# Performance work log

Hardware: AMD Instinct MI355X
Metric: run time of the kernel (lower is better)

The kernel has to match this reference:

```python
import jax, jax.numpy as jnp
import numpy as np

EPS = 1e-5
NEG_SLOPE = 0.01  # torch F.leaky_relu default


def _batchnorm(h, gamma, beta):
    # BatchNorm1d in training mode: batch stats over node dim, biased variance
    mu = jnp.mean(h, axis=0)
    var = jnp.mean((h - mu) ** 2, axis=0)
    return gamma * (h - mu) * jax.lax.rsqrt(var + EPS) + beta


def setup_inputs() -> dict:
    N, E, H, ED = 16384, 524288, 128, 16
    key = jax.random.key(0)
    ks = jax.random.split(key, 12)
    s = 1.0 / np.sqrt(H)
    return {
        "x": jax.random.normal(ks[0], (N, H), jnp.float32),
        "edge_index": jax.random.randint(ks[1], (2, E), 0, N, jnp.int64),
        "edge_attr": jax.random.normal(ks[2], (E, ED), jnp.float32),
        "Wq": jax.random.normal(ks[3], (H, H), jnp.float32) * s,
        "bq": jnp.zeros((H,), jnp.float32),
        "Wk": jax.random.normal(ks[4], (H, H), jnp.float32) * s,
        "bk": jnp.zeros((H,), jnp.float32),
        "Wv": jax.random.normal(ks[5], (H, H), jnp.float32) * s,
        "bv": jnp.zeros((H,), jnp.float32),
        "We": jax.random.normal(ks[6], (ED, 1), jnp.float32) * (1.0 / np.sqrt(ED)),
        "be": jnp.zeros((1,), jnp.float32),
        "bn1_g": jnp.ones((H,), jnp.float32),
        "bn1_b": jnp.zeros((H,), jnp.float32),
        "W1": jax.random.normal(ks[7], (H, 2 * H), jnp.float32) * s,
        "b1": jnp.zeros((2 * H,), jnp.float32),
        "W2": jax.random.normal(ks[8], (2 * H, H), jnp.float32) * (1.0 / np.sqrt(2 * H)),
        "b2": jnp.zeros((H,), jnp.float32),
        "bn2_g": jnp.ones((H,), jnp.float32),
        "bn2_b": jnp.zeros((H,), jnp.float32),
    }


def reference(x, edge_index, edge_attr, Wq, bq, Wk, bk, Wv, bv, We, be,
              bn1_g, bn1_b, W1, b1, W2, b2, bn2_g, bn2_b):
    N = x.shape[0]
    Q = x @ Wq + bq  # [N, H]
    K = x @ Wk + bk
    V = x @ Wv + bv
    Ebias = (edge_attr @ We + be)[:, 0]  # [E], num_heads == 1
    src, dst = edge_index[0], edge_index[1]
    # per-edge dot product over the FULL hidden dim (as in the source)
    scores = jnp.sum(Q[src] * K[dst], axis=1) + Ebias  # [E]
    scores = jnp.where(scores >= 0, scores, NEG_SLOPE * scores)
    # to_dense_adj scatter-adds edge_attr into a dense [N, N] adjacency
    adj = jnp.zeros((N, N), x.dtype).at[src, dst].add(scores)
    attn = jax.nn.softmax(adj, axis=1)  # dense softmax incl. zero non-edges
    x_new = attn @ V  # [N, H]
    h = _batchnorm(x + x_new, bn1_g, bn1_b)
    ffn = jax.nn.relu(h @ W1 + b1) @ W2 + b2
    return _batchnorm(h + ffn, bn2_g, bn2_b)
```

## Files before the change

kernel.cpp:

```cpp
#include <hip/hip_runtime.h>
#include <hip/hip_bf16.h>
#include <math.h>

#define H 128
#define H2 256
#define SLAB 96
#define LDA 136
#define LDA2 264
#define EPS 1e-5f

typedef __attribute__((ext_vector_type(8))) short s16x8;
typedef __attribute__((ext_vector_type(4))) float f32x4;

__device__ __forceinline__ unsigned short f2bf(float f) {
  unsigned u = __float_as_uint(f);
  unsigned r = (u + 0x7FFFu + ((u >> 16) & 1u)) >> 16;
  return (unsigned short)r;
}
__device__ __forceinline__ float bf2f(unsigned short s) {
  return __uint_as_float(((unsigned)s) << 16);
}
__device__ __forceinline__ unsigned short f2h(float f) {
  union { unsigned short s; _Float16 h; } c; c.h = (_Float16)f; return c.s;
}
__device__ __forceinline__ float h2f(unsigned short u) {
  union { unsigned short s; _Float16 h; } c; c.s = u; return (float)c.h;
}

__global__ void wprep(const float* __restrict__ Wq, const float* __restrict__ Wk,
                      const float* __restrict__ Wv, const float* __restrict__ W1,
                      const float* __restrict__ W2,
                      short* qh, short* ql, short* kh, short* kl,
                      short* vh, short* w1h, short* w2h,
                      int* __restrict__ cnt, float* __restrict__ stats, int N)
{
  int job = blockIdx.z;
  if (job == 5) {
    int t = blockIdx.x * 256 + threadIdx.x;
    if (t < N) cnt[t] = 0;
    if (t < 72 * H) stats[t] = 0.f;
    return;
  }
  const float* src; short* dh; short* dl = nullptr; int Kd, Nn;
  if (job == 0)      { src = Wq; dh = qh;  dl = ql; Kd = 128; Nn = 128; }
  else if (job == 1) { src = Wk; dh = kh;  dl = kl; Kd = 128; Nn = 128; }
  else if (job == 2) { src = Wv; dh = vh;           Kd = 128; Nn = 128; }
  else if (job == 3) { src = W1; dh = w1h;          Kd = 128; Nn = 256; }
  else               { src = W2; dh = w2h;          Kd = 256; Nn = 128; }
  int t = blockIdx.x * 256 + threadIdx.x;
  if (t >= Kd * Nn) return;
  int n = t / Kd, k = t - n * Kd;
  float v = src[(size_t)k * Nn + n];
  unsigned short h = f2bf(v);
  dh[t] = (short)h;
  if (dl) dl[t] = (short)f2bf(v - bf2f(h));
}

__global__ __launch_bounds__(256) void ebias(
    const float* __restrict__ ea, const float* __restrict__ We,
    const float* __restrict__ be, float* __restrict__ Eb, int E)
{
  int e = blockIdx.x * 256 + threadIdx.x;
  if (e >= E) return;
  float4 w0 = *(const float4*)&We[0], w1 = *(const float4*)&We[4];
  float4 w2 = *(const float4*)&We[8], w3 = *(const float4*)&We[12];
  const float4* p = (const float4*)&ea[(size_t)e * 16];
  float4 a0 = p[0], a1 = p[1], a2 = p[2], a3 = p[3];
  float s = a0.x * w0.x + a0.y * w0.y + a0.z * w0.z + a0.w * w0.w
          + a1.x * w1.x + a1.y * w1.y + a1.z * w1.z + a1.w * w1.w
          + a2.x * w2.x + a2.y * w2.y + a2.z * w2.z + a2.w * w2.w
          + a3.x * w3.x + a3.y * w3.y + a3.z * w3.z + a3.w * w3.w;
  Eb[e] = s + be[0];
}

__global__ __launch_bounds__(256) void qkv_mfma(
    const float* __restrict__ x,
    const short* __restrict__ Wqh, const short* __restrict__ Wql,
    const short* __restrict__ Wkh, const short* __restrict__ Wkl,
    const short* __restrict__ Wvh,
    const float* __restrict__ bq, const float* __restrict__ bk,
    const float* __restrict__ bv,
    unsigned short* __restrict__ Qh, unsigned short* __restrict__ Kh,
    unsigned short* __restrict__ Vh, float* __restrict__ SVp)
{
  __shared__ __align__(16) short Ahi[64 * LDA];
  __shared__ __align__(16) short Alo[64 * LDA];
  int tid = threadIdx.x;
  int bm = blockIdx.x * 64;
  int wave = tid >> 6, lane = tid & 63;
  int quad = lane >> 4, l16 = lane & 15;
  int wn = wave * 32;

#pragma unroll
  for (int i = 0; i < 4; ++i) {
    int g = i * 256 + tid;
    int row = g >> 4, f = g & 15;
    const float4* xp = (const float4*)&x[(size_t)(bm + row) * H + f * 8];
    float4 v0 = xp[0], v1 = xp[1];
    float vv[8] = {v0.x, v0.y, v0.z, v0.w, v1.x, v1.y, v1.z, v1.w};
    s16x8 hv, lv;
#pragma unroll
    for (int j = 0; j < 8; ++j) {
      unsigned short hh = f2bf(vv[j]);
      hv[j] = (short)hh;
      lv[j] = (short)f2bf(vv[j] - bf2f(hh));
    }
    *(s16x8*)&Ahi[row * LDA + f * 8] = hv;
    *(s16x8*)&Alo[row * LDA + f * 8] = lv;
  }
  __syncthreads();

  for (int ph = 0; ph < 3; ++ph) {
    const short* Bh = (ph == 0) ? Wqh : (ph == 1) ? Wkh : Wvh;
    const short* Bl = (ph == 0) ? Wql : (ph == 1) ? Wkl : nullptr;

    s16x8 bh[2][4], bl2[2][4];
#pragma unroll
    for (int nt = 0; nt < 2; ++nt)
#pragma unroll
      for (int ks = 0; ks < 4; ++ks)
        bh[nt][ks] = *(const s16x8*)&Bh[(size_t)(wn + nt * 16 + l16) * H + ks * 32 + quad * 8];
    if (Bl) {
#pragma unroll
      for (int nt = 0; nt < 2; ++nt)
#pragma unroll
        for (int ks = 0; ks < 4; ++ks)
          bl2[nt][ks] = *(const s16x8*)&Bl[(size_t)(wn + nt * 16 + l16) * H + ks * 32 + quad * 8];
    }

    f32x4 acc[4][2];
#pragma unroll
    for (int mt = 0; mt < 4; ++mt)
#pragma unroll
      for (int nt = 0; nt < 2; ++nt) acc[mt][nt] = (f32x4){0.f, 0.f, 0.f, 0.f};

#pragma unroll
    for (int ks = 0; ks < 4; ++ks) {
      int kof = ks * 32 + quad * 8;
      s16x8 ah[4], al[4];
#pragma unroll
      for (int mt = 0; mt < 4; ++mt) {
        ah[mt] = *(s16x8*)&Ahi[(mt * 16 + l16) * LDA + kof];
        al[mt] = *(s16x8*)&Alo[(mt * 16 + l16) * LDA + kof];
      }
#pragma unroll
      for (int mt = 0; mt < 4; ++mt)
#pragma unroll
        for (int nt = 0; nt < 2; ++nt) {
          acc[mt][nt] = __builtin_amdgcn_mfma_f32_16x16x32_bf16(ah[mt], bh[nt][ks], acc[mt][nt], 0, 0, 0);
          if (ph < 2) {
            acc[mt][nt] = __builtin_amdgcn_mfma_f32_16x16x32_bf16(ah[mt], bl2[nt][ks], acc[mt][nt], 0, 0, 0);
            acc[mt][nt] = __builtin_amdgcn_mfma_f32_16x16x32_bf16(al[mt], bh[nt][ks], acc[mt][nt], 0, 0, 0);
          }
        }
    }

    if (ph == 0) {
#pragma unroll
      for (int nt = 0; nt < 2; ++nt) {
        int col = wn + nt * 16 + l16;
        float bb = bq[col];
#pragma unroll
        for (int mt = 0; mt < 4; ++mt)
#pragma unroll
          for (int r = 0; r < 4; ++r) {
            int row = bm + mt * 16 + quad * 4 + r;
            Qh[(size_t)row * H + col] = f2h(acc[mt][nt][r] + bb);
          }
      }
    } else if (ph == 1) {
#pragma unroll
      for (int nt = 0; nt < 2; ++nt) {
        int col = wn + nt * 16 + l16;
        float bb = bk[col];
#pragma unroll
        for (int mt = 0; mt < 4; ++mt)
#pragma unroll
          for (int r = 0; r < 4; ++r) {
            int row = bm + mt * 16 + quad * 4 + r;
            Kh[(size_t)row * H + col] = f2h(acc[mt][nt][r] + bb);
          }
      }
    } else {
      int bank = blockIdx.x & 7;
#pragma unroll
      for (int nt = 0; nt < 2; ++nt) {
        int col = wn + nt * 16 + l16;
        float bb = bv[col];
        float ps = 0.f;
#pragma unroll
        for (int mt = 0; mt < 4; ++mt)
#pragma unroll
          for (int r = 0; r < 4; ++r) {
            int row = bm + mt * 16 + quad * 4 + r;
            float v = acc[mt][nt][r] + bb;
            Vh[(size_t)row * H + col] = f2h(v);
            ps += v;
          }
        ps += __shfl_xor(ps, 16);
        ps += __shfl_xor(ps, 32);
        if (quad == 0) atomicAdd(&SVp[bank * H + col], ps);
      }
    }
  }
}

__global__ __launch_bounds__(256) void ebfill(
    const int* __restrict__ ei,
    const float* __restrict__ Eb,
    const unsigned short* __restrict__ Qh,
    const unsigned short* __restrict__ Kh,
    int* __restrict__ cnt,
    int2* __restrict__ slabDE, int E, int N)
{
  __shared__ int qeP[2048];
  __shared__ float qeB[2048];
  __shared__ int qn;
  int tid = threadIdx.x;
  int grp = blockIdx.x & 7;
  int blk = blockIdx.x >> 3;
  int lo = grp * (N >> 3), hi = lo + (N >> 3);
  int per = E >> 8;
  int base = blk * per;
  const int* eiD = ei + E;

  if (tid == 0) qn = 0;
  __syncthreads();

  for (int i = 0; i < per; i += 256) {
    int e = base + i + tid;
    if (e >= E) continue;
    int src = ei[e];
    int dst = eiD[e];
    float b = Eb[e];
    if (src >= lo && src < hi) {
      int p = atomicAdd(&qn, 1);
      qeP[p] = (dst << 11) | (src - lo);
      qeB[p] = b;
    }
  }
  __syncthreads();

  int m = qn;
  int sub = tid & 7, st = tid >> 3;
  int j = st;
  for (; j + 32 < m; j += 64) {
    int pA = qeP[j], pB = qeP[j + 32];
    float bA = qeB[j], bB = qeB[j + 32];
    int sA = lo + (pA & 2047), dA = pA >> 11;
    int sB = lo + (pB & 2047), dB = pB >> 11;
    const s16x8* qpA = (const s16x8*)(Qh + (size_t)sA * H);
    const s16x8* kpA = (const s16x8*)(Kh + (size_t)dA * H);
    const s16x8* qpB = (const s16x8*)(Qh + (size_t)sB * H);
    const s16x8* kpB = (const s16x8*)(Kh + (size_t)dB * H);
    s16x8 qa0 = qpA[sub], qb0 = qpA[8 + sub];
    s16x8 ka0 = kpA[sub], kb0 = kpA[8 + sub];
    s16x8 qa1 = qpB[sub], qb1 = qpB[8 + sub];
    s16x8 ka1 = kpB[sub], kb1 = kpB[8 + sub];
    float s0 = 0.f, s1 = 0.f;
#pragma unroll
    for (int u = 0; u < 8; ++u) {
      s0 += h2f((unsigned short)qa0[u]) * h2f((unsigned short)ka0[u]);
      s0 += h2f((unsigned short)qb0[u]) * h2f((unsigned short)kb0[u]);
      s1 += h2f((unsigned short)qa1[u]) * h2f((unsigned short)ka1[u]);
      s1 += h2f((unsigned short)qb1[u]) * h2f((unsigned short)kb1[u]);
    }
    s0 += __shfl_xor(s0, 1); s1 += __shfl_xor(s1, 1);
    s0 += __shfl_xor(s0, 2); s1 += __shfl_xor(s1, 2);
    s0 += __shfl_xor(s0, 4); s1 += __shfl_xor(s1, 4);
    if (sub == 0) {
      s0 += bA; s1 += bB;
      s0 = (s0 >= 0.f) ? s0 : 0.01f * s0;
      s1 = (s1 >= 0.f) ? s1 : 0.01f * s1;
      int posA = atomicAdd(&cnt[sA], 1);
      if (posA < SLAB) {
        int2 rec; rec.x = dA; rec.y = __float_as_int(s0);
        slabDE[sA * SLAB + posA] = rec;
      }
      int posB = atomicAdd(&cnt[sB], 1);
      if (posB < SLAB) {
        int2 rec; rec.x = dB; rec.y = __float_as_int(s1);
        slabDE[sB * SLAB + posB] = rec;
      }
    }
  }
  for (; j < m; j += 32) {
    int p = qeP[j];
    float b = qeB[j];
    int src = lo + (p & 2047), dst = p >> 11;
    const s16x8* qp = (const s16x8*)(Qh + (size_t)src * H);
    const s16x8* kp = (const s16x8*)(Kh + (size_t)dst * H);
    s16x8 qa = qp[sub], qb = qp[8 + sub];
    s16x8 ka = kp[sub], kb = kp[8 + sub];
    float s = 0.f;
#pragma unroll
    for (int u = 0; u < 8; ++u) {
      s += h2f((unsigned short)qa[u]) * h2f((unsigned short)ka[u]);
      s += h2f((unsigned short)qb[u]) * h2f((unsigned short)kb[u]);
    }
    s += __shfl_xor(s, 1);
    s += __shfl_xor(s, 2);
    s += __shfl_xor(s, 4);
    if (sub == 0) {
      s += b;
      s = (s >= 0.f) ? s : 0.01f * s;
      int pos = atomicAdd(&cnt[src], 1);
      if (pos < SLAB) {
        int2 rec; rec.x = dst; rec.y = __float_as_int(s);
        slabDE[src * SLAB + pos] = rec;
      }
    }
  }
}

__global__ __launch_bounds__(256) void attn_fused(
    const float* __restrict__ x,
    const unsigned short* __restrict__ Vh,
    const float* __restrict__ SVp, const int* __restrict__ cnt,
    const int2* __restrict__ slabDE,
    float* __restrict__ h1, float* __restrict__ sum1p, float* __restrict__ sq1p,
    int N)
{
  __shared__ float sv[4][SLAB];
  __shared__ int sd[4][SLAB];
  __shared__ short sown[4][SLAB];
  __shared__ float csum[H], csq[H];
  int tid = threadIdx.x;
  int team = tid >> 6, lane = tid & 63;
  int i = blockIdx.x * 4 + team;
  int k = cnt[i]; if (k > SLAB) k = SLAB;
  int base = i * SLAB;

  if (tid < H) { csum[tid] = 0.f; csq[tid] = 0.f; }
  __syncthreads();

  for (int p = lane; p < k; p += 64) {
    int2 de = slabDE[base + p];
    sd[team][p] = de.x;
    sv[team][p] = __int_as_float(de.y);
  }

  for (int p = lane; p < k; p += 64) {
    int d = sd[team][p];
    int o = p;
    for (int q = p - 1; q >= 0; --q)
      o = (sd[team][q] == d) ? q : o;
    sown[team][p] = (short)o;
  }
  for (int p = lane; p < k; p += 64) {
    int o = sown[team][p];
    if (o != p) atomicAdd(&sv[team][o], sv[team][p]);
  }

  float mx = 0.f;
  for (int p = lane; p < k; p += 64)
    if (sown[team][p] == (short)p) mx = fmaxf(mx, sv[team][p]);
#pragma unroll
  for (int msk = 32; msk; msk >>= 1) mx = fmaxf(mx, __shfl_xor(mx, msk));
  float em = __expf(-mx);

  float zl = 0.f;
  for (int p = lane; p < k; p += 64) {
    float cf = 0.f;
    if (sown[team][p] == (short)p) cf = __expf(sv[team][p] - mx) - em;
    sv[team][p] = cf;
    zl += cf;
  }
#pragma unroll
  for (int msk = 32; msk; msk >>= 1) zl += __shfl_xor(zl, msk);
  float Zi = 1.f / ((float)N * em + zl);

  float sx = 0.f, sy = 0.f;
#pragma unroll
  for (int b = 0; b < 8; ++b) {
    float2 t = *(const float2*)&SVp[b * H + lane * 2];
    sx += t.x; sy += t.y;
  }

  const ushort2* V2 = (const ushort2*)Vh;
  float ax = em * sx, ay = em * sy;
  int c = 0;
  for (; c + 8 <= k; c += 8) {
    float cf[8]; int dd[8]; ushort2 vv[8];
#pragma unroll
    for (int u = 0; u < 8; ++u) { cf[u] = sv[team][c + u]; dd[u] = sd[team][c + u]; }
#pragma unroll
    for (int u = 0; u < 8; ++u) vv[u] = V2[(size_t)dd[u] * 64 + lane];
#pragma unroll
    for (int u = 0; u < 8; ++u) {
      ax += cf[u] * h2f(vv[u].x);
      ay += cf[u] * h2f(vv[u].y);
    }
  }
  for (; c < k; ++c) {
    float cf = sv[team][c];
    ushort2 v0 = V2[(size_t)sd[team][c] * 64 + lane];
    ax += cf * h2f(v0.x); ay += cf * h2f(v0.y);
  }
  float2 xx = *(const float2*)&x[(size_t)i * H + lane * 2];
  float ox = xx.x + ax * Zi;
  float oy = xx.y + ay * Zi;
  float2 ov; ov.x = ox; ov.y = oy;
  *(float2*)&h1[(size_t)i * H + lane * 2] = ov;

  int c0 = lane * 2;
  atomicAdd(&csum[c0 + 0], ox); atomicAdd(&csq[c0 + 0], ox * ox);
  atomicAdd(&csum[c0 + 1], oy); atomicAdd(&csq[c0 + 1], oy * oy);
  __syncthreads();
  if (tid < H) {
    int bank = blockIdx.x & 15;
    atomicAdd(&sum1p[bank * H + tid], csum[tid]);
    atomicAdd(&sq1p[bank * H + tid], csq[tid]);
  }
}

__global__ __launch_bounds__(256) void ffn_fused(
    const float* __restrict__ h1, const short* __restrict__ W1h,
    const float* __restrict__ b1, const short* __restrict__ W2h,
    const float* __restrict__ b2,
    const float* __restrict__ sum1p, const float* __restrict__ sq1p,
    const float* __restrict__ g1, const float* __restrict__ bb1,
    float* __restrict__ h2, float* __restrict__ sum2p, float* __restrict__ sq2p,
    float invN)
{
  __shared__ __align__(16) short As[32 * LDA];
  __shared__ __align__(16) short Ts[32 * LDA2];
  __shared__ float aF[H], bF[H];
  int tid = threadIdx.x;
  int bm = blockIdx.x * 32;
  int wave = tid >> 6, lane = tid & 63;
  int quad = lane >> 4, l16 = lane & 15;

  if (tid < H) {
    float s = 0.f, q = 0.f;
#pragma unroll
    for (int b = 0; b < 16; ++b) { s += sum1p[b * H + tid]; q += sq1p[b * H + tid]; }
    float mu = s * invN;
    float var = q * invN - mu * mu;
    float rs = rsqrtf(var + EPS);
    float a = g1[tid] * rs;
    aF[tid] = a;
    bF[tid] = bb1[tid] - a * mu;
  }
  __syncthreads();

  int f = tid & 15;
#pragma unroll
  for (int i = 0; i < 2; ++i) {
    int g = i * 256 + tid;
    int row = g >> 4;
    const float4* xp = (const float4*)&h1[(size_t)(bm + row) * H + f * 8];
    float4 v0 = xp[0], v1 = xp[1];
    float vv[8] = {v0.x, v0.y, v0.z, v0.w, v1.x, v1.y, v1.z, v1.w};
    s16x8 hv;
#pragma unroll
    for (int j = 0; j < 8; ++j) {
      int c = f * 8 + j;
      hv[j] = (short)f2bf(aF[c] * vv[j] + bF[c]);
    }
    *(s16x8*)&As[row * LDA + f * 8] = hv;
  }

  int wn1 = wave * 64;
  s16x8 b1f[4][4];
#pragma unroll
  for (int nt = 0; nt < 4; ++nt)
#pragma unroll
    for (int ks = 0; ks < 4; ++ks)
      b1f[nt][ks] = *(const s16x8*)&W1h[(size_t)(wn1 + nt * 16 + l16) * H + ks * 32 + quad * 8];
  __syncthreads();

  f32x4 acc1[2][4];
#pragma unroll
  for (int mt = 0; mt < 2; ++mt)
#pragma unroll
    for (int nt = 0; nt < 4; ++nt) acc1[mt][nt] = (f32x4){0.f, 0.f, 0.f, 0.f};

#pragma unroll
  for (int ks = 0; ks < 4; ++ks) {
    int kof = ks * 32 + quad * 8;
    s16x8 ah[2];
#pragma unroll
    for (int mt = 0; mt < 2; ++mt) ah[mt] = *(s16x8*)&As[(mt * 16 + l16) * LDA + kof];
#pragma unroll
    for (int mt = 0; mt < 2; ++mt)
#pragma unroll
      for (int nt = 0; nt < 4; ++nt)
        acc1[mt][nt] = __builtin_amdgcn_mfma_f32_16x16x32_bf16(ah[mt], b1f[nt][ks], acc1[mt][nt], 0, 0, 0);
  }

#pragma unroll
  for (int nt = 0; nt < 4; ++nt) {
    int col = wn1 + nt * 16 + l16;
    float bb = b1[col];
#pragma unroll
    for (int mt = 0; mt < 2; ++mt)
#pragma unroll
      for (int r = 0; r < 4; ++r) {
        int row = mt * 16 + quad * 4 + r;
        float v = acc1[mt][nt][r] + bb;
        v = v > 0.f ? v : 0.f;
        Ts[row * LDA2 + col] = (short)f2bf(v);
      }
  }

  int wn2 = wave * 32;
  s16x8 b2f[2][8];
#pragma unroll
  for (int nt = 0; nt < 2; ++nt)
#pragma unroll
    for (int ks = 0; ks < 8; ++ks)
      b2f[nt][ks] = *(const s16x8*)&W2h[(size_t)(wn2 + nt * 16 + l16) * H2 + ks * 32 + quad * 8];
  __syncthreads();

  f32x4 acc2[2][2];
#pragma unroll
  for (int mt = 0; mt < 2; ++mt)
#pragma unroll
    for (int nt = 0; nt < 2; ++nt) acc2[mt][nt] = (f32x4){0.f, 0.f, 0.f, 0.f};

#pragma unroll
  for (int ks = 0; ks < 8; ++ks) {
    int kof = ks * 32 + quad * 8;
    s16x8 ah[2];
#pragma unroll
    for (int mt = 0; mt < 2; ++mt) ah[mt] = *(s16x8*)&Ts[(mt * 16 + l16) * LDA2 + kof];
#pragma unroll
    for (int mt = 0; mt < 2; ++mt)
#pragma unroll
      for (int nt = 0; nt < 2; ++nt)
        acc2[mt][nt] = __builtin_amdgcn_mfma_f32_16x16x32_bf16(ah[mt], b2f[nt][ks], acc2[mt][nt], 0, 0, 0);
  }

  int bank = blockIdx.x & 15;
#pragma unroll
  for (int nt = 0; nt < 2; ++nt) {
    int col = wn2 + nt * 16 + l16;
    float ra = aF[col], rb = bF[col];
    float bb = b2[col];
    float ps = 0.f, pq = 0.f;
#pragma unroll
    for (int mt = 0; mt < 2; ++mt)
#pragma unroll
      for (int r = 0; r < 4; ++r) {
        int row = bm + mt * 16 + quad * 4 + r;
        float rr = ra * h1[(size_t)row * H + col] + rb;
        float v = acc2[mt][nt][r] + bb + rr;
        h2[(size_t)row * H + col] = v;
        ps += v; pq += v * v;
      }
    ps += __shfl_xor(ps, 16); ps += __shfl_xor(ps, 32);
    pq += __shfl_xor(pq, 16); pq += __shfl_xor(pq, 32);
    if (quad == 0) {
      atomicAdd(&sum2p[bank * H + col], ps);
      atomicAdd(&sq2p[bank * H + col], pq);
    }
  }
}

__global__ __launch_bounds__(256) void bn_apply(
    const float* __restrict__ X,
    const float* __restrict__ sum2p, const float* __restrict__ sq2p,
    const float* __restrict__ g2, const float* __restrict__ bb2,
    float* __restrict__ Y, size_t n4, float invN)
{
  __shared__ float A2s[H], B2s[H];
  int tid = threadIdx.x;
  if (tid < H) {
    float s = 0.f, q = 0.f;
#pragma unroll
    for (int b = 0; b < 16; ++b) { s += sum2p[b * H + tid]; q += sq2p[b * H + tid]; }
    float mu = s * invN;
    float var = q * invN - mu * mu;
    float rs = rsqrtf(var + EPS);
    float a = g2[tid] * rs;
    A2s[tid] = a;
    B2s[tid] = bb2[tid] - a * mu;
  }
  __syncthreads();
  size_t i = (size_t)blockIdx.x * blockDim.x + tid;
  if (i >= n4) return;
  float4 v = ((const float4*)X)[i];
  int c = (int)((i * 4) & (H - 1));
  float4 a = *(const float4*)&A2s[c];
  float4 b = *(const float4*)&B2s[c];
  v.x = a.x * v.x + b.x; v.y = a.y * v.y + b.y;
  v.z = a.z * v.z + b.z; v.w = a.w * v.w + b.w;
  ((float4*)Y)[i] = v;
}

extern "C" void kernel_launch(void* const* d_in, const int* in_sizes, int n_in,
                              void* d_out, int out_size, void* d_ws, size_t ws_size,
                              hipStream_t stream)
{
  const float* x  = (const float*)d_in[0];
  const int*   ei = (const int*)d_in[1];
  const float* ea = (const float*)d_in[2];
  const float* Wq = (const float*)d_in[3];
  const float* bq = (const float*)d_in[4];
  const float* Wk = (const float*)d_in[5];
  const float* bk = (const float*)d_in[6];
  const float* Wv = (const float*)d_in[7];
  const float* bv = (const float*)d_in[8];
  const float* We = (const float*)d_in[9];
  const float* be = (const float*)d_in[10];
  const float* g1 = (const float*)d_in[11];
  const float* bb1 = (const float*)d_in[12];
  const float* W1 = (const float*)d_in[13];
  const float* b1 = (const float*)d_in[14];
  const float* W2 = (const float*)d_in[15];
  const float* b2 = (const float*)d_in[16];
  const float* g2 = (const float*)d_in[17];
  const float* bb2 = (const float*)d_in[18];

  int N = in_sizes[0] / H;
  int E = in_sizes[2] / 16;
  size_t NH = (size_t)N * H;
  float invN = 1.0f / (float)N;

  unsigned short* Qh = (unsigned short*)d_ws;
  unsigned short* Kh = Qh + NH;
  unsigned short* Vh = Kh + NH;
  float* h1  = (float*)(Vh + NH);
  int2*  slabDE = (int2*)(h1 + NH);
  int*   cnt    = (int*)(slabDE + (size_t)N * SLAB);
  float* stats  = (float*)(cnt + N);
  float* SVp   = stats;
  float* sum1p = stats + 8 * H;
  float* sq1p  = sum1p + 16 * H;
  float* sum2p = sq1p + 16 * H;
  float* sq2p  = sum2p + 16 * H;
  float* statsEnd = sq2p + 16 * H;
  short* wbuf = (short*)statsEnd;
  short* Wqh = wbuf;
  short* Wql = Wqh + 16384;
  short* Wkh = Wql + 16384;
  short* Wkl = Wkh + 16384;
  short* Wvh = Wkl + 16384;
  short* W1h = Wvh + 16384;
  short* W2h = W1h + 32768;
  float* Eb  = (float*)(W2h + 32768);
  float* h2 = (float*)Qh;

  wprep<<<dim3(128, 1, 6), 256, 0, stream>>>(Wq, Wk, Wv, W1, W2,
      Wqh, Wql, Wkh, Wkl, Wvh, W1h, W2h, cnt, stats, N);

  ebias<<<dim3((E + 255) / 256), 256, 0, stream>>>(ea, We, be, Eb, E);

  qkv_mfma<<<dim3(N / 64), 256, 0, stream>>>(
      x, Wqh, Wql, Wkh, Wkl, Wvh, bq, bk, bv, Qh, Kh, Vh, SVp);

  ebfill<<<dim3(2048), 256, 0, stream>>>(ei, Eb, Qh, Kh, cnt, slabDE, E, N);

  attn_fused<<<dim3(N / 4), 256, 0, stream>>>(x, Vh, SVp, cnt, slabDE,
                                              h1, sum1p, sq1p, N);

  ffn_fused<<<dim3(N / 32), 256, 0, stream>>>(h1, W1h, b1, W2h, b2,
      sum1p, sq1p, g1, bb1, h2, sum2p, sq2p, invN);

  bn_apply<<<dim3((int)((NH / 4 + 255) / 256)), 256, 0, stream>>>(
      h2, sum2p, sq2p, g2, bb2, (float*)d_out, NH / 4, invN);
}
```

Baseline: 226.5 us.

## Use fp16 single-pass QKV MFMA, fold ebias into qkv launch, remap attn blocks

Replaces the split-bf16 (hi/lo, three MFMAs per tile) QKV projection with a single fp16 MFMA pass, removing the low-part weight buffers and the extra LDS tile. It also merges the edge-bias kernel into the QKV launch as extra blocks, saving one kernel launch. Separately, the attention kernel's block-to-node mapping is interleaved into 8 groups, which changes the order in which nodes are visited. The fp16 path lowers precision compared with the bf16x3 emulation, which risks accuracy in the attention scores.

```diff
diff --git a/kernel.cpp b/kernel.cpp
--- a/kernel.cpp
+++ b/kernel.cpp
@@ -30,8 +30,7 @@
 __global__ void wprep(const float* __restrict__ Wq, const float* __restrict__ Wk,
                       const float* __restrict__ Wv, const float* __restrict__ W1,
                       const float* __restrict__ W2,
-                      short* qh, short* ql, short* kh, short* kl,
-                      short* vh, short* w1h, short* w2h,
+                      short* qh, short* kh, short* vh, short* w1h, short* w2h,
                       int* __restrict__ cnt, float* __restrict__ stats, int N)
 {
   int job = blockIdx.z;
@@ -41,51 +40,50 @@
     if (t < 72 * H) stats[t] = 0.f;
     return;
   }
-  const float* src; short* dh; short* dl = nullptr; int Kd, Nn;
-  if (job == 0)      { src = Wq; dh = qh;  dl = ql; Kd = 128; Nn = 128; }
-  else if (job == 1) { src = Wk; dh = kh;  dl = kl; Kd = 128; Nn = 128; }
-  else if (job == 2) { src = Wv; dh = vh;           Kd = 128; Nn = 128; }
-  else if (job == 3) { src = W1; dh = w1h;          Kd = 128; Nn = 256; }
-  else               { src = W2; dh = w2h;          Kd = 256; Nn = 128; }
+  const float* src; short* dh; int Kd, Nn; bool ashalf;
+  if (job == 0)      { src = Wq; dh = qh;  Kd = 128; Nn = 128; ashalf = true; }
+  else if (job == 1) { src = Wk; dh = kh;  Kd = 128; Nn = 128; ashalf = true; }
+  else if (job == 2) { src = Wv; dh = vh;  Kd = 128; Nn = 128; ashalf = true; }
+  else if (job == 3) { src = W1; dh = w1h; Kd = 128; Nn = 256; ashalf = false; }
+  else               { src = W2; dh = w2h; Kd = 256; Nn = 128; ashalf = false; }
   int t = blockIdx.x * 256 + threadIdx.x;
   if (t >= Kd * Nn) return;
   int n = t / Kd, k = t - n * Kd;
   float v = src[(size_t)k * Nn + n];
-  unsigned short h = f2bf(v);
-  dh[t] = (short)h;
-  if (dl) dl[t] = (short)f2bf(v - bf2f(h));
-}
-
-__global__ __launch_bounds__(256) void ebias(
-    const float* __restrict__ ea, const float* __restrict__ We,
-    const float* __restrict__ be, float* __restrict__ Eb, int E)
-{
-  int e = blockIdx.x * 256 + threadIdx.x;
-  if (e >= E) return;
-  float4 w0 = *(const float4*)&We[0], w1 = *(const float4*)&We[4];
-  float4 w2 = *(const float4*)&We[8], w3 = *(const float4*)&We[12];
-  const float4* p = (const float4*)&ea[(size_t)e * 16];
-  float4 a0 = p[0], a1 = p[1], a2 = p[2], a3 = p[3];
-  float s = a0.x * w0.x + a0.y * w0.y + a0.z * w0.z + a0.w * w0.w
-          + a1.x * w1.x + a1.y * w1.y + a1.z * w1.z + a1.w * w1.w
-          + a2.x * w2.x + a2.y * w2.y + a2.z * w2.z + a2.w * w2.w
-          + a3.x * w3.x + a3.y * w3.y + a3.z * w3.z + a3.w * w3.w;
-  Eb[e] = s + be[0];
+  dh[t] = ashalf ? (short)f2h(v) : (short)f2bf(v);
 }
 
 __global__ __launch_bounds__(256) void qkv_mfma(
     const float* __restrict__ x,
-    const short* __restrict__ Wqh, const short* __restrict__ Wql,
-    const short* __restrict__ Wkh, const short* __restrict__ Wkl,
+    const short* __restrict__ Wqh, const short* __restrict__ Wkh,
     const short* __restrict__ Wvh,
     const float* __restrict__ bq, const float* __restrict__ bk,
     const float* __restrict__ bv,
     unsigned short* __restrict__ Qh, unsigned short* __restrict__ Kh,
-    unsigned short* __restrict__ Vh, float* __restrict__ SVp)
+    unsigned short* __restrict__ Vh, float* __restrict__ SVp,
+    const float* __restrict__ ea, const float* __restrict__ We,
+    const float* __restrict__ be, float* __restrict__ Eb,
+    int E, int nqkv)
 {
-  __shared__ __align__(16) short Ahi[64 * LDA];
-  __shared__ __align__(16) short Alo[64 * LDA];
+  __shared__ __align__(16) short A[64 * LDA];
   int tid = threadIdx.x;
+
+  if (blockIdx.x >= nqkv) {
+    int e = (blockIdx.x - nqkv) * 256 + tid;
+    if (e < E) {
+      float4 w0 = *(const float4*)&We[0], w1 = *(const float4*)&We[4];
+      float4 w2 = *(const float4*)&We[8], w3 = *(const float4*)&We[12];
+      const float4* p = (const float4*)&ea[(size_t)e * 16];
+      float4 a0 = p[0], a1 = p[1], a2 = p[2], a3 = p[3];
+      float s = a0.x * w0.x + a0.y * w0.y + a0.z * w0.z + a0.w * w0.w
+              + a1.x * w1.x + a1.y * w1.y + a1.z * w1.z + a1.w * w1.w
+              + a2.x * w2.x + a2.y * w2.y + a2.z * w2.z + a2.w * w2.w
+              + a3.x * w3.x + a3.y * w3.y + a3.z * w3.z + a3.w * w3.w;
+      Eb[e] = s + be[0];
+    }
+    return;
+  }
+
   int bm = blockIdx.x * 64;
   int wave = tid >> 6, lane = tid & 63;
   int quad = lane >> 4, l16 = lane & 15;
@@ -98,35 +96,22 @@
     const float4* xp = (const float4*)&x[(size_t)(bm + row) * H + f * 8];
     float4 v0 = xp[0], v1 = xp[1];
     float vv[8] = {v0.x, v0.y, v0.z, v0.w, v1.x, v1.y, v1.z, v1.w};
-    s16x8 hv, lv;
-#pragma unroll
-    for (int j = 0; j < 8; ++j) {
-      unsigned short hh = f2bf(vv[j]);
-      hv[j] = (short)hh;
-      lv[j] = (short)f2bf(vv[j] - bf2f(hh));
-    }
-    *(s16x8*)&Ahi[row * LDA + f * 8] = hv;
-    *(s16x8*)&Alo[row * LDA + f * 8] = lv;
+    s16x8 hv;
+#pragma unroll
+    for (int j = 0; j < 8; ++j) hv[j] = (short)f2h(vv[j]);
+    *(s16x8*)&A[row * LDA + f * 8] = hv;
   }
   __syncthreads();
 
   for (int ph = 0; ph < 3; ++ph) {
     const short* Bh = (ph == 0) ? Wqh : (ph == 1) ? Wkh : Wvh;
-    const short* Bl = (ph == 0) ? Wql : (ph == 1) ? Wkl : nullptr;
-
-    s16x8 bh[2][4], bl2[2][4];
+
+    s16x8 bh[2][4];
 #pragma unroll
     for (int nt = 0; nt < 2; ++nt)
 #pragma unroll
       for (int ks = 0; ks < 4; ++ks)
         bh[nt][ks] = *(const s16x8*)&Bh[(size_t)(wn + nt * 16 + l16) * H + ks * 32 + quad * 8];
-    if (Bl) {
-#pragma unroll
-      for (int nt = 0; nt < 2; ++nt)
-#pragma unroll
-        for (int ks = 0; ks < 4; ++ks)
-          bl2[nt][ks] = *(const s16x8*)&Bl[(size_t)(wn + nt * 16 + l16) * H + ks * 32 + quad * 8];
-    }
 
     f32x4 acc[4][2];
 #pragma unroll
@@ -137,22 +122,15 @@
 #pragma unroll
     for (int ks = 0; ks < 4; ++ks) {
       int kof = ks * 32 + quad * 8;
-      s16x8 ah[4], al[4];
-#pragma unroll
-      for (int mt = 0; mt < 4; ++mt) {
-        ah[mt] = *(s16x8*)&Ahi[(mt * 16 + l16) * LDA + kof];
-        al[mt] = *(s16x8*)&Alo[(mt * 16 + l16) * LDA + kof];
-      }
+      s16x8 ah[4];
 #pragma unroll
       for (int mt = 0; mt < 4; ++mt)
-#pragma unroll
-        for (int nt = 0; nt < 2; ++nt) {
-          acc[mt][nt] = __builtin_amdgcn_mfma_f32_16x16x32_bf16(ah[mt], bh[nt][ks], acc[mt][nt], 0, 0, 0);
-          if (ph < 2) {
-            acc[mt][nt] = __builtin_amdgcn_mfma_f32_16x16x32_bf16(ah[mt], bl2[nt][ks], acc[mt][nt], 0, 0, 0);
-            acc[mt][nt] = __builtin_amdgcn_mfma_f32_16x16x32_bf16(al[mt], bh[nt][ks], acc[mt][nt], 0, 0, 0);
-          }
-        }
+        ah[mt] = *(s16x8*)&A[(mt * 16 + l16) * LDA + kof];
+#pragma unroll
+      for (int mt = 0; mt < 4; ++mt)
+#pragma unroll
+        for (int nt = 0; nt < 2; ++nt)
+          acc[mt][nt] = __builtin_amdgcn_mfma_f32_16x16x32_f16(ah[mt], bh[nt][ks], acc[mt][nt], 0, 0, 0);
     }
 
     if (ph == 0) {
@@ -327,7 +305,9 @@
   __shared__ float csum[H], csq[H];
   int tid = threadIdx.x;
   int team = tid >> 6, lane = tid & 63;
-  int i = blockIdx.x * 4 + team;
+  int grp = blockIdx.x & 7;
+  int r = blockIdx.x >> 3;
+  int i = grp * (N >> 3) + r * 4 + team;
   int k = cnt[i]; if (k > SLAB) k = SLAB;
   int base = i * SLAB;
 
@@ -632,23 +612,23 @@
   float* sq2p  = sum2p + 16 * H;
   float* statsEnd = sq2p + 16 * H;
   short* wbuf = (short*)statsEnd;
-  short* Wqh = wbuf;
-  short* Wql = Wqh + 16384;
-  short* Wkh = Wql + 16384;
-  short* Wkl = Wkh + 16384;
-  short* Wvh = Wkl + 16384;
-  short* W1h = Wvh + 16384;
+  short* Wqf = wbuf;
+  short* Wkf = Wqf + 16384;
+  short* Wvf = Wkf + 16384;
+  short* W1h = Wvf + 16384;
   short* W2h = W1h + 32768;
   float* Eb  = (float*)(W2h + 32768);
   float* h2 = (float*)Qh;
 
+  int nqkv = N / 64;
+  int nebias = (E + 255) / 256;
+
   wprep<<<dim3(128, 1, 6), 256, 0, stream>>>(Wq, Wk, Wv, W1, W2,
-      Wqh, Wql, Wkh, Wkl, Wvh, W1h, W2h, cnt, stats, N);
-
-  ebias<<<dim3((E + 255) / 256), 256, 0, stream>>>(ea, We, be, Eb, E);
-
-  qkv_mfma<<<dim3(N / 64), 256, 0, stream>>>(
-      x, Wqh, Wql, Wkh, Wkl, Wvh, bq, bk, bv, Qh, Kh, Vh, SVp);
+      Wqf, Wkf, Wvf, W1h, W2h, cnt, stats, N);
+
+  qkv_mfma<<<dim3(nqkv + nebias), 256, 0, stream>>>(
+      x, Wqf, Wkf, Wvf, bq, bk, bv, Qh, Kh, Vh, SVp,
+      ea, We, be, Eb, E, nqkv);
 
   ebfill<<<dim3(2048), 256, 0, stream>>>(ei, Eb, Qh, Kh, cnt, slabDE, E, N);
 
```

New measurement: 219.5 us. 3.1% less time.
